# Performance work log

Hardware: AMD Instinct MI355X
Metric: run time of the kernel (lower is better)

## Reference

```python
import jax, jax.numpy as jnp
import numpy as np

N_EVENTS = 16384   # original pixel events
D = 128            # input_size
H = 128            # hidden_size
K = 9              # kernel 3x3 -> patch coords
S = 2048           # number of patch sequences
LMAX = 108         # max sequence length
T = 147456         # total patch events = sum(lengths) = 9 * N_EVENTS


def setup_inputs() -> dict:
    key = jax.random.key(0)
    ks = jax.random.split(key, 8)
    events = jax.random.normal(ks[0], (N_EVENTS, D), jnp.float32)
    pos_id = jax.random.randint(ks[1], (T,), 0, K, dtype=jnp.int32)
    orig_event_idx = jax.random.randint(ks[2], (T,), 0, N_EVENTS, dtype=jnp.int32)
    # alternating 36/108 lengths: 1024*36 + 1024*108 = 147456 = T
    lengths = jnp.where(jnp.arange(S) % 2 == 0, 36, 108).astype(jnp.int32)
    std = float(np.sqrt(2.0 / (D + H)))
    scatter_w = jax.random.normal(ks[3], (K, H, D), jnp.float32) * std
    gather_w = jax.random.normal(ks[4], (K, H, H), jnp.float32) * std
    lstm_std = float(1.0 / np.sqrt(H))
    w_ih = jax.random.uniform(ks[5], (4 * H, H), jnp.float32, -lstm_std, lstm_std)
    w_hh = jax.random.uniform(ks[6], (4 * H, H), jnp.float32, -lstm_std, lstm_std)
    ln_g = jnp.ones((H,), jnp.float32)
    ln_b = jnp.zeros((H,), jnp.float32)
    return dict(events=events, scatter_w=scatter_w, gather_w=gather_w,
                w_ih=w_ih, w_hh=w_hh, ln_g=ln_g, ln_b=ln_b,
                pos_id=pos_id, orig_event_idx=orig_event_idx, lengths=lengths)


def _pos_proj(x, W, pos_id):
    # position-indexed projection: out[t] = W[pos_id[t]] @ x[t]
    # loop over small fixed K=9 with masked accumulate (matches the torch loop)
    out = jnp.zeros((x.shape[0], W.shape[1]), x.dtype)
    for k in range(W.shape[0]):
        out = out + jnp.where((pos_id == k)[:, None], x @ W[k].T, 0.0)
    return out


def reference(events, scatter_w, gather_w, w_ih, w_hh, ln_g, ln_b,
              pos_id, orig_event_idx, lengths):
    # scatter events to patch replicas
    x = events[orig_event_idx]                           # [T, D]
    x = _pos_proj(x, scatter_w, pos_id)                  # [T, H]

    # flat (sequence-major) -> padded [S, LMAX, H]
    seq_offsets = jnp.cumsum(lengths) - lengths          # [S]
    seq_ids = jnp.repeat(jnp.arange(S), lengths, total_repeat_length=T)
    pos_in_seq = jnp.arange(T) - seq_offsets[seq_ids]
    padded = jnp.zeros((S, LMAX, H), x.dtype).at[seq_ids, pos_in_seq].set(x)

    # single-layer bias-free LSTM (pytorch gate order i, f, g, o), zero init.
    # zero-padding after each sequence's valid region leaves valid outputs
    # identical to a PackedSequence LSTM.
    def step(carry, xt):                                 # xt: [S, H]
        h, c = carry
        gates = xt @ w_ih.T + h @ w_hh.T                 # [S, 4H]
        i, f, g, o = jnp.split(gates, 4, axis=-1)
        c = jax.nn.sigmoid(f) * c + jax.nn.sigmoid(i) * jnp.tanh(g)
        h = jax.nn.sigmoid(o) * jnp.tanh(c)
        return (h, c), h

    init = (jnp.zeros((S, H), x.dtype), jnp.zeros((S, H), x.dtype))
    _, hs = jax.lax.scan(step, init, jnp.swapaxes(padded, 0, 1))  # [LMAX, S, H]
    o_flat = jnp.swapaxes(hs, 0, 1)[seq_ids, pos_in_seq]          # [T, H]

    o_flat = _pos_proj(o_flat, gather_w, pos_id)                  # [T, H]

    # gather patch events back to pixel events (scatter-add) + residual + LN
    out = jnp.zeros((N_EVENTS, H), x.dtype).at[orig_event_idx].add(o_flat)
    out = out + events                                   # input_proj is None (D == H)
    mu = jnp.mean(out, axis=-1, keepdims=True)
    var = jnp.var(out, axis=-1, keepdims=True)
    out = (out - mu) * jax.lax.rsqrt(var + 1e-5) * ln_g + ln_b
    return out
```

## Files before the change

### kernel.cpp

```cpp
#include <hip/hip_runtime.h>

#define N_EVENTS 16384
#define DIM 128
#define NK 9
#define NSEQ 2048
#define TT 147456
#define CHUNK 64
#define NCHUNK_MAX (TT/CHUNK + NK)
#define NHBLK 576

typedef __attribute__((ext_vector_type(8))) short bf16x8;
typedef __attribute__((ext_vector_type(4))) float f32x4;
typedef __attribute__((ext_vector_type(4))) int i32x4;
typedef __attribute__((ext_vector_type(2))) int i32x2;

#define OFF_EV     0UL
#define OFF_WC     (OFF_EV   + (size_t)N_EVENTS*DIM*2)
#define OFF_SCAT   (OFF_WC   + (size_t)512*256*2)
#define OFF_GATH   (OFF_SCAT + (size_t)NK*DIM*DIM*2)
#define OFF_XS     (OFF_GATH + (size_t)NK*DIM*DIM*2)
#define OFF_HS     (OFF_XS   + (size_t)TT*DIM*2)
#define OFF_KLIST  (OFF_HS   + (size_t)TT*DIM*2)
#define OFF_ECNT   (OFF_KLIST+ (size_t)TT*4)
#define OFF_EOFF   (OFF_ECNT + 16384UL*4)
#define OFF_ECNT2  (OFF_EOFF + 16392UL*4)
#define OFF_ELIST  (OFF_ECNT2+ 16384UL*4)
#define OFF_SEQOFF (OFF_ELIST+ (size_t)TT*4)
#define OFF_GROUP  (OFF_SEQOFF + (size_t)NSEQ*4)
#define OFF_MISC   (OFF_GROUP  + (size_t)NSEQ*4)
#define OFF_BH     (OFF_MISC   + 256UL)

__device__ __forceinline__ short f2b(float f) {
    union { float f; unsigned u; } v; v.f = f;
    unsigned r = (v.u + 0x7FFFu + ((v.u >> 16) & 1u)) >> 16;
    return (short)r;
}
__device__ __forceinline__ float asf(unsigned u) {
    union { unsigned u; float f; } v; v.u = u; return v.f;
}
__device__ __forceinline__ float fsig(float x) {
    return __builtin_amdgcn_rcpf(1.f + __expf(-x));
}
__device__ __forceinline__ float ftanh(float x) {
    return 1.f - 2.f * __builtin_amdgcn_rcpf(__expf(2.f * x) + 1.f);
}

__device__ __forceinline__ float plo(float a, float b) {
    i32x2 r = __builtin_amdgcn_permlane32_swap(__float_as_int(a), __float_as_int(b),
                                               false, false);
    return __int_as_float(r[0]);
}
__device__ __forceinline__ float phi(float a, float b) {
    i32x2 r = __builtin_amdgcn_permlane32_swap(__float_as_int(a), __float_as_int(b),
                                               false, false);
    return __int_as_float(r[1]);
}

__device__ __forceinline__ void mfma_vab(f32x4& c, bf16x8 a, bf16x8 b) {
    asm("v_mfma_f32_16x16x32_bf16 %0, %1, %2, %0" : "+v"(c) : "v"(a), "a"(b));
}
#define MFA(c, a, b) mfma_vab(c, a, b);

__device__ __forceinline__ void wg_bar_nodrain() {
    __builtin_amdgcn_sched_barrier(0);
    asm volatile("s_waitcnt lgkmcnt(0)");
    __builtin_amdgcn_s_barrier();
    __builtin_amdgcn_sched_barrier(0);
}

__global__ void convert_kernel(const float* __restrict__ ev, const float* __restrict__ wih,
                               const float* __restrict__ whh, const float* __restrict__ sw,
                               const float* __restrict__ gw,
                               short* __restrict__ evb, short* __restrict__ wcb,
                               short* __restrict__ swb, short* __restrict__ gwb,
                               int* __restrict__ ecnt, int* __restrict__ ecnt2) {
    int idx = blockIdx.x * blockDim.x + threadIdx.x;
    if (idx < N_EVENTS * DIM) evb[idx] = f2b(ev[idx]);
    if (idx < 512 * DIM) {
        int j = idx >> 7, d = idx & 127;
        wcb[j * 256 + d]       = f2b(wih[idx]);
        wcb[j * 256 + 128 + d] = f2b(whh[idx]);
    }
    if (idx < NK * DIM * DIM) { swb[idx] = f2b(sw[idx]); gwb[idx] = f2b(gw[idx]); }
    if (idx < N_EVENTS) { ecnt[idx] = 0; ecnt2[idx] = 0; }
}

__global__ void hist_kernel(const int* __restrict__ pos, const int* __restrict__ orig,
                            int* __restrict__ blockhist, int* __restrict__ ecnt) {
    __shared__ int h[NK];
    int tid = threadIdx.x;
    if (tid < NK) h[tid] = 0;
    __syncthreads();
    int t = blockIdx.x * 256 + tid;
    atomicAdd(&h[pos[t]], 1);
    atomicAdd(&ecnt[orig[t]], 1);
    __syncthreads();
    if (tid < NK) blockhist[blockIdx.x * NK + tid] = h[tid];
}

__global__ void plan_kernel(int* __restrict__ blockhist, int* __restrict__ misc,
                            const int* __restrict__ lengths, int* __restrict__ seq_off,
                            int* __restrict__ grouped,
                            const int* __restrict__ ecnt, int* __restrict__ eoff) {
    int tid = threadIdx.x;
    if (blockIdx.x == 0) {
        __shared__ int h[NHBLK * NK];
        for (int i = tid; i < NHBLK * NK; i += 256) h[i] = blockhist[i];
        __syncthreads();
        if (tid < NK) {
            int run = 0;
            for (int b = 0; b < NHBLK; b++) {
                int v = h[b * NK + tid];
                h[b * NK + tid] = run;
                run += v;
            }
            misc[tid] = run;
        }
        __syncthreads();
        if (tid == 0) {
            int ko = 0, co = 0;
            for (int k = 0; k < NK; k++) {
                int c = misc[k];
                misc[32 + k] = ko;
                misc[48 + k] = co;
                ko += c;
                co += (c + CHUNK - 1) / CHUNK;
            }
            misc[48 + NK] = co;
        }
        __syncthreads();
        for (int i = tid; i < NHBLK * NK; i += 256) blockhist[i] = h[i];
    } else if (blockIdx.x == 1) {
        __shared__ int lens[NSEQ];
        __shared__ int tsum[256], tlong[256];
        for (int i = tid; i < NSEQ; i += 256) lens[i] = lengths[i];
        __syncthreads();
        int base = tid * 8;
        int ls[8]; int s = 0, lc = 0;
        #pragma unroll
        for (int i = 0; i < 8; i++) { ls[i] = lens[base + i]; s += ls[i]; lc += (ls[i] > 64) ? 1 : 0; }
        tsum[tid] = s; tlong[tid] = lc;
        __syncthreads();
        for (int d = 1; d < 256; d <<= 1) {
            int a = (tid >= d) ? tsum[tid - d] : 0;
            int b = (tid >= d) ? tlong[tid - d] : 0;
            __syncthreads();
            tsum[tid] += a; tlong[tid] += b;
            __syncthreads();
        }
        int nlong_total = tlong[255];
        int excl = tsum[tid] - s;
        int excl_long = tlong[tid] - lc;
        int run = 0, runl = 0;
        #pragma unroll
        for (int i = 0; i < 8; i++) {
            int sid = base + i;
            seq_off[sid] = excl + run;
            int lb = excl_long + runl;
            if (ls[i] > 64) { grouped[lb] = sid; runl++; }
            else            { grouped[nlong_total + (sid - lb)] = sid; }
            run += ls[i];
        }
    } else {
        __shared__ int part[256];
        int base = tid * 64;
        int s = 0;
        for (int j = 0; j < 64; j++) s += ecnt[base + j];
        part[tid] = s;
        __syncthreads();
        for (int d = 1; d < 256; d <<= 1) {
            int a = (tid >= d) ? part[tid - d] : 0;
            __syncthreads();
            part[tid] += a;
            __syncthreads();
        }
        int run = part[tid] - s;
        for (int j = 0; j < 64; j++) {
            eoff[base + j] = run;
            run += ecnt[base + j];
        }
        if (tid == 255) eoff[N_EVENTS] = run;
    }
}

__global__ void fill_kernel(const int* __restrict__ pos, const int* __restrict__ orig,
                            const int* __restrict__ blockhist, const int* __restrict__ misc,
                            int* __restrict__ klist,
                            const int* __restrict__ eoff, int* __restrict__ ecnt2,
                            int* __restrict__ elist) {
    __shared__ int off[NK];
    int tid = threadIdx.x;
    if (tid < NK) off[tid] = misc[32 + tid] + blockhist[blockIdx.x * NK + tid];
    __syncthreads();
    int t = blockIdx.x * 256 + tid;
    int p = atomicAdd(&off[pos[t]], 1);
    klist[p] = t;
    int o = orig[t];
    int p2 = atomicAdd(&ecnt2[o], 1);
    elist[eoff[o] + p2] = t;
}

__global__ void bucket_gemm(const short* __restrict__ src, const short* __restrict__ wall,
                            const int* __restrict__ klist, const int* __restrict__ misc,
                            const int* __restrict__ orig, short* __restrict__ rows_out,
                            int mode) {
    const int* chunkoff = misc + 48;
    int b = blockIdx.x;
    if (b >= chunkoff[NK]) return;
    int k = 0;
    while (k < NK - 1 && chunkoff[k + 1] <= b) k++;
    int lc = b - chunkoff[k];
    int cnt = misc[k];
    int base = misc[32 + k] + lc * CHUNK;
    int nv = min(CHUNK, cnt - lc * CHUNK);

    __shared__ int tok[CHUNK], ridx[CHUNK];
    __shared__ short A[CHUNK * 136];
    int tid = threadIdx.x;
    if (tid < CHUNK) {
        int tv = klist[base + ((tid < nv) ? tid : 0)];
        tok[tid] = tv;
        ridx[tid] = (mode == 0) ? orig[tv] : tv;
    }
    __syncthreads();
    {
        int row = tid >> 2, part = tid & 3;
        const i32x4* s4 = (const i32x4*)(src + (size_t)ridx[row] * DIM + part * 32);
        i32x4* d4 = (i32x4*)(A + row * 136 + part * 32);
        d4[0] = s4[0]; d4[1] = s4[1]; d4[2] = s4[2]; d4[3] = s4[3];
    }
    __syncthreads();
    int wave = tid >> 6, lane = tid & 63, l15 = lane & 15, q = lane >> 4;
    const short* wk = wall + (size_t)k * DIM * DIM;
    bf16x8 Bf[2][4];
    #pragma unroll
    for (int nt = 0; nt < 2; nt++) {
        int h = wave * 32 + nt * 16 + l15;
        #pragma unroll
        for (int kt = 0; kt < 4; kt++)
            Bf[nt][kt] = *(const bf16x8*)(wk + h * DIM + kt * 32 + q * 8);
    }
    f32x4 C[4][2];
    #pragma unroll
    for (int mt = 0; mt < 4; mt++)
        #pragma unroll
        for (int nt = 0; nt < 2; nt++) C[mt][nt] = (f32x4){0.f, 0.f, 0.f, 0.f};
    #pragma unroll
    for (int mt = 0; mt < 4; mt++) {
        bf16x8 Afr[4];
        const short* ar = A + (mt * 16 + l15) * 136 + q * 8;
        Afr[0] = *(const bf16x8*)(ar);
        Afr[1] = *(const bf16x8*)(ar + 32);
        Afr[2] = *(const bf16x8*)(ar + 64);
        Afr[3] = *(const bf16x8*)(ar + 96);
        #pragma unroll
        for (int nt = 0; nt < 2; nt++)
            #pragma unroll
            for (int kt = 0; kt < 4; kt++)
                C[mt][nt] = __builtin_amdgcn_mfma_f32_16x16x32_bf16(Afr[kt], Bf[nt][kt], C[mt][nt], 0, 0, 0);
    }
    __syncthreads();
    #pragma unroll
    for (int mt = 0; mt < 4; mt++)
        #pragma unroll
        for (int nt = 0; nt < 2; nt++)
            #pragma unroll
            for (int r = 0; r < 4; r++) {
                int row = mt * 16 + q * 4 + r;
                int col = wave * 32 + nt * 16 + l15;
                A[row * 136 + col] = f2b(C[mt][nt][r]);
            }
    __syncthreads();
    {
        int row = tid >> 2, part = tid & 3;
        if (row < nv) {
            const i32x4* s4 = (const i32x4*)(A + row * 136 + part * 32);
            i32x4* d4 = (i32x4*)(rows_out + (size_t)tok[row] * DIM + part * 32);
            d4[0] = s4[0]; d4[1] = s4[1]; d4[2] = s4[2]; d4[3] = s4[3];
        }
    }
}

#define TAIL(IDX, SEL, SLOT) { \
    float iA = SEL(Ci[0], Ci[2]), iB = SEL(Ci[1], Ci[3]); \
    float fA = SEL(Cf[0], Cf[2]), fB = SEL(Cf[1], Cf[3]); \
    float gA = SEL(Cg[0], Cg[2]), gB = SEL(Cg[1], Cg[3]); \
    float oA = SEL(Co[0], Co[2]), oB = SEL(Co[1], Co[3]); \
    if ((IDX) < lenA) { \
        float si = fsig(iA), sf = fsig(fA), so = fsig(oA); \
        float tg = ftanh(gA); \
        float cn = sf * cA + si * tg; \
        float th = ftanh(cn); \
        cA = cn; \
        hb[(SLOT) * 1088 + rowA * 136 + u] = f2b(so * th); \
    } \
    if ((IDX) < lenB) { \
        float si = fsig(iB), sf = fsig(fB), so = fsig(oB); \
        float tg = ftanh(gB); \
        float cn = sf * cB + si * tg; \
        float th = ftanh(cn); \
        cB = cn; \
        hb[(SLOT) * 1088 + rowB * 136 + u] = f2b(so * th); \
    } \
}

#define LSTM_G(J2, PF) { \
    const int i2 = ib8 + 2 * (J2); \
    f32x4 Ci = {0.f,0.f,0.f,0.f}, Cf = {0.f,0.f,0.f,0.f}; \
    f32x4 Cg = {0.f,0.f,0.f,0.f}, Co = {0.f,0.f,0.f,0.f}; \
    MFA(Ci, PF[0], Bf[0][0]) MFA(Cf, PF[0], Bf[1][0]) \
    MFA(Cg, PF[0], Bf[2][0]) MFA(Co, PF[0], Bf[3][0]) \
    MFA(Ci, PF[1], Bf[0][1]) MFA(Cf, PF[1], Bf[1][1]) \
    MFA(Cg, PF[1], Bf[2][1]) MFA(Co, PF[1], Bf[3][1]) \
    MFA(Ci, PF[2], Bf[0][2]) MFA(Cf, PF[2], Bf[1][2]) \
    MFA(Cg, PF[2], Bf[2][2]) MFA(Co, PF[2], Bf[3][2]) \
    MFA(Ci, PF[3], Bf[0][3]) MFA(Cf, PF[3], Bf[1][3]) \
    MFA(Cg, PF[3], Bf[2][3]) MFA(Co, PF[3], Bf[3][3]) \
     \
    bf16x8 He0, He1, He2, He3; \
    { const short* hp_ = b0 + (lo8 ? (((2*(J2)+7)&7) * 1088) : 8704); \
      He0 = *(const bf16x8*)(hp_);      He1 = *(const bf16x8*)(hp_ + 32); \
      He2 = *(const bf16x8*)(hp_ + 64); He3 = *(const bf16x8*)(hp_ + 96); } \
    MFA(Ci, He0, Bf[0][4]) MFA(Cf, He0, Bf[1][4]) \
    MFA(Cg, He0, Bf[2][4]) MFA(Co, He0, Bf[3][4]) \
    MFA(Ci, He1, Bf[0][5]) MFA(Cf, He1, Bf[1][5]) \
    MFA(Cg, He1, Bf[2][5]) MFA(Co, He1, Bf[3][5]) \
    MFA(Ci, He2, Bf[0][6]) MFA(Cf, He2, Bf[1][6]) \
    MFA(Cg, He2, Bf[2][6]) MFA(Co, He2, Bf[3][6]) \
    MFA(Ci, He3, Bf[0][7]) MFA(Cf, He3, Bf[1][7]) \
    MFA(Cg, He3, Bf[2][7]) MFA(Co, He3, Bf[3][7]) \
    TAIL(i2, plo, (2*(J2)) & 7) \
    wg_bar_nodrain(); \
     \
    bf16x8 Ho0, Ho1, Ho2, Ho3; \
    { const short* hp_ = b0 + (lo8 ? 8704 : (((2*(J2)) & 7) * 1088)); \
      Ho0 = *(const bf16x8*)(hp_);      Ho1 = *(const bf16x8*)(hp_ + 32); \
      Ho2 = *(const bf16x8*)(hp_ + 64); Ho3 = *(const bf16x8*)(hp_ + 96); } \
    MFA(Ci, Ho0, Bf[0][4]) MFA(Cf, Ho0, Bf[1][4]) \
    MFA(Cg, Ho0, Bf[2][4]) MFA(Co, Ho0, Bf[3][4]) \
    MFA(Ci, Ho1, Bf[0][5]) MFA(Cf, Ho1, Bf[1][5]) \
    MFA(Cg, Ho1, Bf[2][5]) MFA(Co, Ho1, Bf[3][5]) \
    MFA(Ci, Ho2, Bf[0][6]) MFA(Cf, Ho2, Bf[1][6]) \
    MFA(Cg, Ho2, Bf[2][6]) MFA(Co, Ho2, Bf[3][6]) \
    MFA(Ci, Ho3, Bf[0][7]) MFA(Cf, Ho3, Bf[1][7]) \
    MFA(Cg, Ho3, Bf[2][7]) MFA(Co, Ho3, Bf[3][7]) \
     \
    { const short* xp_ = xs + xoff; \
      PF[0] = *(const bf16x8*)(xp_);      PF[1] = *(const bf16x8*)(xp_ + 32); \
      PF[2] = *(const bf16x8*)(xp_ + 64); PF[3] = *(const bf16x8*)(xp_ + 96); } \
    xoff += ((i2 + 6 + loff) < my_len) ? 2 * DIM : 0; \
    TAIL(i2 + 1, phi, (2*(J2)+1) & 7) \
    wg_bar_nodrain(); \
}

__global__ __launch_bounds__(512)
__attribute__((amdgpu_waves_per_eu(2, 2)))
void lstm_kernel(
        const short* __restrict__ xs, const short* __restrict__ wc,
        short* __restrict__ hstore, const int* __restrict__ seq_off,
        const int* __restrict__ grouped, const int* __restrict__ lengths) {
    __shared__ int s_off[8], s_len[8];
    __shared__ short hchunk[11][8][136];
    int tid = threadIdx.x;
    if (tid < 8) {
        int s = grouped[blockIdx.x * 8 + tid];
        s_off[tid] = seq_off[s];
        s_len[tid] = lengths[s];
    }
    for (int j = tid; j < 11 * 8 * 136; j += 512) ((short*)hchunk)[j] = 0;
    __syncthreads();
    int lane = tid & 63, l15 = lane & 15, ql = lane >> 4;
    int wave = tid >> 6;
    int u = wave * 16 + l15;
    short* hb = (short*)hchunk;
    bf16x8 Bf[4][8];
    #pragma unroll
    for (int g = 0; g < 4; g++) {
        int j = g * 128 + u;
        #pragma unroll
        for (int kt = 0; kt < 8; kt++)
            Bf[g][kt] = *(const bf16x8*)(wc + j * 256 + kt * 32 + ql * 8);
    }
    int maxlen = 0;
    #pragma unroll
    for (int i = 0; i < 8; i++) maxlen = max(maxlen, s_len[i]);
    int sq = l15 & 7;
    int loff = l15 >> 3;
    bool lo8 = (l15 < 8);
    int my_off = s_off[sq];
    int my_len = s_len[sq];
    const short* b0 = hb + sq * 136 + ql * 8;
    int rowA = (ql < 2) ? (ql * 4 + 0) : ((ql - 2) * 4 + 2);
    int rowB = (ql < 2) ? (ql * 4 + 1) : ((ql - 2) * 4 + 3);
    int lenA = s_len[rowA], lenB = s_len[rowB];
    float cA = 0.f, cB = 0.f;
    bf16x8 Pf0[4], Pf1[4];
    int xoff = (my_off + loff) * DIM + ql * 8;
    {
        const short* xp = xs + xoff;
        Pf0[0] = *(const bf16x8*)(xp);      Pf0[1] = *(const bf16x8*)(xp + 32);
        Pf0[2] = *(const bf16x8*)(xp + 64); Pf0[3] = *(const bf16x8*)(xp + 96);
        const short* xq = xp + 2 * DIM;
        Pf1[0] = *(const bf16x8*)(xq);      Pf1[1] = *(const bf16x8*)(xq + 32);
        Pf1[2] = *(const bf16x8*)(xq + 64); Pf1[3] = *(const bf16x8*)(xq + 96);
    }
    xoff += 4 * DIM;

    int nb8 = (maxlen + 7) >> 3;
    for (int ob = 0; ob < nb8; ob++) {
        int ib8 = ob * 8;
        LSTM_G(0, Pf0)
        LSTM_G(1, Pf1)
        LSTM_G(2, Pf0)
        LSTM_G(3, Pf1)
        #pragma unroll
        for (int it = 0; it < 2; it++) {
            int idx = tid + it * 512;
            int st = idx >> 7, s = (idx >> 4) & 7, part = idx & 15;
            int ig = ib8 + st;
            if (ig < s_len[s]) {
                i32x4 v = *(const i32x4*)&hchunk[st][s][part * 8];
                *(i32x4*)(hstore + (size_t)(s_off[s] + ig) * DIM + part * 8) = v;
            }
        }
        wg_bar_nodrain();
    }
}

__global__ void gather_ln(const short* __restrict__ of, const int* __restrict__ eoff,
                          const int* __restrict__ elist, const float* __restrict__ ev,
                          const float* __restrict__ g, const float* __restrict__ bta,
                          float* __restrict__ out) {
    int tid = threadIdx.x;
    int wave = tid >> 6, lane = tid & 63;
    int e = blockIdx.x * 4 + wave;
    int s0 = eoff[e], s1 = eoff[e + 1];
    float x0 = 0.f, x1 = 0.f;
    for (int j = s0; j < s1; j++) {
        int t = elist[j];
        unsigned v = *(const unsigned*)(of + (size_t)t * DIM + lane * 2);
        x0 += asf(v << 16);
        x1 += asf(v & 0xffff0000u);
    }
    const float2* e2 = (const float2*)(ev + (size_t)e * DIM);
    float2 evv = e2[lane];
    x0 += evv.x; x1 += evv.y;
    float sm = x0 + x1, sq = x0 * x0 + x1 * x1;
    #pragma unroll
    for (int m = 1; m < 64; m <<= 1) {
        sm += __shfl_xor(sm, m, 64);
        sq += __shfl_xor(sq, m, 64);
    }
    float mean = sm * (1.f / DIM);
    float var = sq * (1.f / DIM) - mean * mean;
    float rs = rsqrtf(var + 1e-5f);
    float2 gv = ((const float2*)g)[lane], bv = ((const float2*)bta)[lane];
    float2 ov;
    ov.x = (x0 - mean) * rs * gv.x + bv.x;
    ov.y = (x1 - mean) * rs * gv.y + bv.y;
    ((float2*)(out + (size_t)e * DIM))[lane] = ov;
}

extern "C" void kernel_launch(void* const* d_in, const int* in_sizes, int n_in,
                              void* d_out, int out_size, void* d_ws, size_t ws_size,
                              hipStream_t stream) {
    const float* events = (const float*)d_in[0];
    const float* scat   = (const float*)d_in[1];
    const float* gath   = (const float*)d_in[2];
    const float* wih    = (const float*)d_in[3];
    const float* whh    = (const float*)d_in[4];
    const float* lng    = (const float*)d_in[5];
    const float* lnb    = (const float*)d_in[6];
    const int* posid    = (const int*)d_in[7];
    const int* orig     = (const int*)d_in[8];
    const int* lens     = (const int*)d_in[9];
    char* ws = (char*)d_ws;
    short* evb   = (short*)(ws + OFF_EV);
    short* wcb   = (short*)(ws + OFF_WC);
    short* swb   = (short*)(ws + OFF_SCAT);
    short* gwb   = (short*)(ws + OFF_GATH);
    short* xs    = (short*)(ws + OFF_XS);
    short* hs    = (short*)(ws + OFF_HS);
    int*   klist = (int*)(ws + OFF_KLIST);
    int*   ecnt  = (int*)(ws + OFF_ECNT);
    int*   eoff  = (int*)(ws + OFF_EOFF);
    int*   ecnt2 = (int*)(ws + OFF_ECNT2);
    int*   elist = (int*)(ws + OFF_ELIST);
    int*   seqo  = (int*)(ws + OFF_SEQOFF);
    int*   grp   = (int*)(ws + OFF_GROUP);
    int*   misc  = (int*)(ws + OFF_MISC);
    int*   bh    = (int*)(ws + OFF_BH);
    float* out   = (float*)d_out;

    convert_kernel<<<8192, 256, 0, stream>>>(events, wih, whh, scat, gath,
                                             evb, wcb, swb, gwb, ecnt, ecnt2);
    hist_kernel<<<NHBLK, 256, 0, stream>>>(posid, orig, bh, ecnt);
    plan_kernel<<<3, 256, 0, stream>>>(bh, misc, lens, seqo, grp, ecnt, eoff);
    fill_kernel<<<NHBLK, 256, 0, stream>>>(posid, orig, bh, misc, klist, eoff, ecnt2, elist);
    bucket_gemm<<<NCHUNK_MAX, 256, 0, stream>>>(evb, swb, klist, misc, orig, xs, 0);
    lstm_kernel<<<256, 512, 0, stream>>>(xs, wcb, hs, seqo, grp, lens);
    bucket_gemm<<<NCHUNK_MAX, 256, 0, stream>>>(hs, gwb, klist, misc, orig, xs, 1);
    gather_ln<<<4096, 256, 0, stream>>>(xs, eoff, elist, events, lng, lnb, out);
}
```

Baseline: 288.0 us.

## Fuse preprocessing kernels into one persistent kernel with grid barriers

Merges the convert, histogram, plan and fill kernels into a single 576-block kernel that separates its phases with atomic-counter grid barriers, with a memset added to reset the barrier counters. This removes three kernel launches and their launch gaps. The cost is grid-wide spin barriers, which depend on all 576 blocks being co-resident. It also changes the LSTM's wg_bar_nodrain from sched_barrier to memory clobbers, which may alter instruction scheduling in the recurrent loop.

```diff
diff --git a/kernel.cpp b/kernel.cpp
--- a/kernel.cpp
+++ b/kernel.cpp
@@ -8,6 +8,7 @@
 #define CHUNK 64
 #define NCHUNK_MAX (TT/CHUNK + NK)
 #define NHBLK 576
+#define PREP_BLOCKS 576
 
 typedef __attribute__((ext_vector_type(8))) short bf16x8;
 typedef __attribute__((ext_vector_type(4))) float f32x4;
@@ -62,56 +63,74 @@
 #define MFA(c, a, b) mfma_vab(c, a, b);
 
 __device__ __forceinline__ void wg_bar_nodrain() {
-    __builtin_amdgcn_sched_barrier(0);
-    asm volatile("s_waitcnt lgkmcnt(0)");
+    asm volatile("s_waitcnt lgkmcnt(0)" ::: "memory");
     __builtin_amdgcn_s_barrier();
-    __builtin_amdgcn_sched_barrier(0);
-}
-
-__global__ void convert_kernel(const float* __restrict__ ev, const float* __restrict__ wih,
-                               const float* __restrict__ whh, const float* __restrict__ sw,
-                               const float* __restrict__ gw,
-                               short* __restrict__ evb, short* __restrict__ wcb,
-                               short* __restrict__ swb, short* __restrict__ gwb,
-                               int* __restrict__ ecnt, int* __restrict__ ecnt2) {
-    int idx = blockIdx.x * blockDim.x + threadIdx.x;
-    if (idx < N_EVENTS * DIM) evb[idx] = f2b(ev[idx]);
-    if (idx < 512 * DIM) {
+    asm volatile("" ::: "memory");
+}
+
+__device__ __forceinline__ void gridbar(unsigned* c, unsigned n) {
+    __syncthreads();
+    __threadfence();
+    if (threadIdx.x == 0) {
+        __hip_atomic_fetch_add(c, 1u, __ATOMIC_ACQ_REL, __HIP_MEMORY_SCOPE_AGENT);
+        while (__hip_atomic_load(c, __ATOMIC_ACQUIRE, __HIP_MEMORY_SCOPE_AGENT) < n)
+            __builtin_amdgcn_s_sleep(16);
+    }
+    __syncthreads();
+    __threadfence();
+}
+
+__global__ __launch_bounds__(256) void prep_kernel(
+        const float* __restrict__ ev, const float* __restrict__ wih,
+        const float* __restrict__ whh, const float* __restrict__ sw,
+        const float* __restrict__ gw,
+        short* __restrict__ evb, short* __restrict__ wcb,
+        short* __restrict__ swb, short* __restrict__ gwb,
+        int* __restrict__ ecnt, int* __restrict__ ecnt2,
+        const int* __restrict__ pos, const int* __restrict__ orig,
+        int* __restrict__ blockhist, int* __restrict__ misc,
+        const int* __restrict__ lengths, int* __restrict__ seq_off,
+        int* __restrict__ grouped, int* __restrict__ eoff,
+        int* __restrict__ klist, int* __restrict__ elist,
+        unsigned* __restrict__ bar) {
+    __shared__ int smem[NHBLK * NK];
+    int tid = threadIdx.x;
+    int b = blockIdx.x;
+    int gidx = b * 256 + tid;
+    const int GSTRIDE = PREP_BLOCKS * 256;
+
+    for (int idx = gidx; idx < N_EVENTS * DIM; idx += GSTRIDE) evb[idx] = f2b(ev[idx]);
+    for (int idx = gidx; idx < 512 * DIM; idx += GSTRIDE) {
         int j = idx >> 7, d = idx & 127;
         wcb[j * 256 + d]       = f2b(wih[idx]);
         wcb[j * 256 + 128 + d] = f2b(whh[idx]);
     }
-    if (idx < NK * DIM * DIM) { swb[idx] = f2b(sw[idx]); gwb[idx] = f2b(gw[idx]); }
-    if (idx < N_EVENTS) { ecnt[idx] = 0; ecnt2[idx] = 0; }
-}
-
-__global__ void hist_kernel(const int* __restrict__ pos, const int* __restrict__ orig,
-                            int* __restrict__ blockhist, int* __restrict__ ecnt) {
-    __shared__ int h[NK];
-    int tid = threadIdx.x;
-    if (tid < NK) h[tid] = 0;
-    __syncthreads();
-    int t = blockIdx.x * 256 + tid;
-    atomicAdd(&h[pos[t]], 1);
-    atomicAdd(&ecnt[orig[t]], 1);
-    __syncthreads();
-    if (tid < NK) blockhist[blockIdx.x * NK + tid] = h[tid];
-}
-
-__global__ void plan_kernel(int* __restrict__ blockhist, int* __restrict__ misc,
-                            const int* __restrict__ lengths, int* __restrict__ seq_off,
-                            int* __restrict__ grouped,
-                            const int* __restrict__ ecnt, int* __restrict__ eoff) {
-    int tid = threadIdx.x;
-    if (blockIdx.x == 0) {
-        __shared__ int h[NHBLK * NK];
+    for (int idx = gidx; idx < NK * DIM * DIM; idx += GSTRIDE) {
+        swb[idx] = f2b(sw[idx]); gwb[idx] = f2b(gw[idx]);
+    }
+    for (int idx = gidx; idx < N_EVENTS; idx += GSTRIDE) { ecnt[idx] = 0; ecnt2[idx] = 0; }
+    gridbar(bar + 0, PREP_BLOCKS);
+
+    {
+        if (tid < NK) smem[tid] = 0;
+        __syncthreads();
+        int t = b * 256 + tid;
+        atomicAdd(&smem[pos[t]], 1);
+        atomicAdd(&ecnt[orig[t]], 1);
+        __syncthreads();
+        if (tid < NK) blockhist[b * NK + tid] = smem[tid];
+    }
+    gridbar(bar + 1, PREP_BLOCKS);
+
+    if (b == 0) {
+        int* h = smem;
         for (int i = tid; i < NHBLK * NK; i += 256) h[i] = blockhist[i];
         __syncthreads();
         if (tid < NK) {
             int run = 0;
-            for (int b = 0; b < NHBLK; b++) {
-                int v = h[b * NK + tid];
-                h[b * NK + tid] = run;
+            for (int bb = 0; bb < NHBLK; bb++) {
+                int v = h[bb * NK + tid];
+                h[bb * NK + tid] = run;
                 run += v;
             }
             misc[tid] = run;
@@ -130,9 +149,10 @@
         }
         __syncthreads();
         for (int i = tid; i < NHBLK * NK; i += 256) blockhist[i] = h[i];
-    } else if (blockIdx.x == 1) {
-        __shared__ int lens[NSEQ];
-        __shared__ int tsum[256], tlong[256];
+    } else if (b == 1) {
+        int* lens = smem;
+        int* tsum = smem + 2048;
+        int* tlong = smem + 2304;
         for (int i = tid; i < NSEQ; i += 256) lens[i] = lengths[i];
         __syncthreads();
         int base = tid * 8;
@@ -143,9 +163,9 @@
         __syncthreads();
         for (int d = 1; d < 256; d <<= 1) {
             int a = (tid >= d) ? tsum[tid - d] : 0;
-            int b = (tid >= d) ? tlong[tid - d] : 0;
+            int bb = (tid >= d) ? tlong[tid - d] : 0;
             __syncthreads();
-            tsum[tid] += a; tlong[tid] += b;
+            tsum[tid] += a; tlong[tid] += bb;
             __syncthreads();
         }
         int nlong_total = tlong[255];
@@ -161,8 +181,8 @@
             else            { grouped[nlong_total + (sid - lb)] = sid; }
             run += ls[i];
         }
-    } else {
-        __shared__ int part[256];
+    } else if (b == 2) {
+        int* part = smem;
         int base = tid * 64;
         int s = 0;
         for (int j = 0; j < 64; j++) s += ecnt[base + j];
@@ -181,23 +201,18 @@
         }
         if (tid == 255) eoff[N_EVENTS] = run;
     }
-}
-
-__global__ void fill_kernel(const int* __restrict__ pos, const int* __restrict__ orig,
-                            const int* __restrict__ blockhist, const int* __restrict__ misc,
-                            int* __restrict__ klist,
-                            const int* __restrict__ eoff, int* __restrict__ ecnt2,
-                            int* __restrict__ elist) {
-    __shared__ int off[NK];
-    int tid = threadIdx.x;
-    if (tid < NK) off[tid] = misc[32 + tid] + blockhist[blockIdx.x * NK + tid];
-    __syncthreads();
-    int t = blockIdx.x * 256 + tid;
-    int p = atomicAdd(&off[pos[t]], 1);
-    klist[p] = t;
-    int o = orig[t];
-    int p2 = atomicAdd(&ecnt2[o], 1);
-    elist[eoff[o] + p2] = t;
+    gridbar(bar + 2, PREP_BLOCKS);
+
+    {
+        if (tid < NK) smem[tid] = misc[32 + tid] + blockhist[b * NK + tid];
+        __syncthreads();
+        int t = b * 256 + tid;
+        int p = atomicAdd(&smem[pos[t]], 1);
+        klist[p] = t;
+        int o = orig[t];
+        int p2 = atomicAdd(&ecnt2[o], 1);
+        elist[eoff[o] + p2] = t;
+    }
 }
 
 __global__ void bucket_gemm(const short* __restrict__ src, const short* __restrict__ wall,
@@ -316,7 +331,6 @@
     MFA(Cg, PF[2], Bf[2][2]) MFA(Co, PF[2], Bf[3][2]) \
     MFA(Ci, PF[3], Bf[0][3]) MFA(Cf, PF[3], Bf[1][3]) \
     MFA(Cg, PF[3], Bf[2][3]) MFA(Co, PF[3], Bf[3][3]) \
-     \
     bf16x8 He0, He1, He2, He3; \
     { const short* hp_ = b0 + (lo8 ? (((2*(J2)+7)&7) * 1088) : 8704); \
       He0 = *(const bf16x8*)(hp_);      He1 = *(const bf16x8*)(hp_ + 32); \
@@ -331,7 +345,6 @@
     MFA(Cg, He3, Bf[2][7]) MFA(Co, He3, Bf[3][7]) \
     TAIL(i2, plo, (2*(J2)) & 7) \
     wg_bar_nodrain(); \
-     \
     bf16x8 Ho0, Ho1, Ho2, Ho3; \
     { const short* hp_ = b0 + (lo8 ? 8704 : (((2*(J2)) & 7) * 1088)); \
       Ho0 = *(const bf16x8*)(hp_);      Ho1 = *(const bf16x8*)(hp_ + 32); \
@@ -344,7 +357,6 @@
     MFA(Cg, Ho2, Bf[2][6]) MFA(Co, Ho2, Bf[3][6]) \
     MFA(Ci, Ho3, Bf[0][7]) MFA(Cf, Ho3, Bf[1][7]) \
     MFA(Cg, Ho3, Bf[2][7]) MFA(Co, Ho3, Bf[3][7]) \
-     \
     { const short* xp_ = xs + xoff; \
       PF[0] = *(const bf16x8*)(xp_);      PF[1] = *(const bf16x8*)(xp_ + 32); \
       PF[2] = *(const bf16x8*)(xp_ + 64); PF[3] = *(const bf16x8*)(xp_ + 96); } \
@@ -490,13 +502,14 @@
     int*   grp   = (int*)(ws + OFF_GROUP);
     int*   misc  = (int*)(ws + OFF_MISC);
     int*   bh    = (int*)(ws + OFF_BH);
+    unsigned* bar = (unsigned*)(ws + OFF_MISC + 240);
     float* out   = (float*)d_out;
 
-    convert_kernel<<<8192, 256, 0, stream>>>(events, wih, whh, scat, gath,
-                                             evb, wcb, swb, gwb, ecnt, ecnt2);
-    hist_kernel<<<NHBLK, 256, 0, stream>>>(posid, orig, bh, ecnt);
-    plan_kernel<<<3, 256, 0, stream>>>(bh, misc, lens, seqo, grp, ecnt, eoff);
-    fill_kernel<<<NHBLK, 256, 0, stream>>>(posid, orig, bh, misc, klist, eoff, ecnt2, elist);
+    hipMemsetAsync(bar, 0, 12, stream);
+    prep_kernel<<<PREP_BLOCKS, 256, 0, stream>>>(
+        events, wih, whh, scat, gath, evb, wcb, swb, gwb,
+        ecnt, ecnt2, posid, orig, bh, misc, lens, seqo, grp, eoff,
+        klist, elist, bar);
     bucket_gemm<<<NCHUNK_MAX, 256, 0, stream>>>(evb, swb, klist, misc, orig, xs, 0);
     lstm_kernel<<<256, 512, 0, stream>>>(xs, wcb, hs, seqo, grp, lens);
     bucket_gemm<<<NCHUNK_MAX, 256, 0, stream>>>(hs, gwb, klist, misc, orig, xs, 1);
```

Result: slower. 684.8 us (+137.8%).
